# Performance work log

Measured on AMD Instinct MI355X. Metric: run time of the kernel, lower is better.

Reference implementation:

```python
import jax, jax.numpy as jnp
import numpy as np
import math

N = 200000      # active voxels
M = 100000      # matched in/out pairs per kernel offset
K = 27          # kernel volume (3x3x3)
CIN = 32
COUT = 64


def setup_inputs() -> dict:
    key = jax.random.key(0)
    k1, k2, k3, k4, k5 = jax.random.split(key, 5)
    input_feat = jax.random.normal(k1, (N, CIN), dtype=jnp.float32)
    input_coord = jax.random.randint(k2, (N, 4), 0, 1024, dtype=jnp.int32)
    input_cmap = jax.random.randint(k3, (N,), 0, N, dtype=jnp.int32)
    input_kmap = jax.random.randint(k4, (K, M, 2), 0, N, dtype=jnp.int32)
    std = 1.0 / math.sqrt(CIN * K)  # reset_parameters: uniform(-std, std)
    kw, kb = jax.random.split(k5)
    kernel = jax.random.uniform(kw, (K, CIN, COUT), dtype=jnp.float32,
                                minval=-std, maxval=std)
    bias = jax.random.uniform(kb, (COUT,), dtype=jnp.float32,
                              minval=-std, maxval=std)
    return {"input_feat": input_feat, "input_coord": input_coord,
            "input_cmap": input_cmap, "input_kmap": input_kmap,
            "kernel": kernel, "bias": bias}


def reference(input_feat, input_coord, input_cmap, input_kmap, kernel, bias):
    # Sparse 3D conv, stride=1: output coords == input coords, n_out = N.
    # For each kernel offset k, the kmap gives (in_idx, out_idx) pairs:
    #   out[out_idx] += in[in_idx] @ kernel[k]
    n_out = input_feat.shape[0]
    in_idx = input_kmap[..., 0]           # [K, M]
    out_idx = input_kmap[..., 1]          # [K, M]
    gathered = input_feat[in_idx]         # [K, M, CIN]  (gather)
    contrib = jnp.einsum('kmi,kio->kmo', gathered, kernel)  # per-offset GEMM
    out = jnp.zeros((n_out, kernel.shape[-1]), dtype=input_feat.dtype)
    out = out.at[out_idx.reshape(-1)].add(contrib.reshape(-1, kernel.shape[-1]))
    out = out + bias
    return out
```

## Files before the change

kernel.cpp:

```cpp
#include <hip/hip_runtime.h>
#include <stdint.h>

#define KVOL 27
#define CIN  32
#define COUT 64
#define RB16 16
#define WPG  4
#define ENTCAP 640
#define SCAN_CHUNK 4096

typedef __attribute__((ext_vector_type(8))) short bf16x8;
typedef __attribute__((ext_vector_type(4))) float f32x4;

__device__ __forceinline__ ushort f2bf(float f) {
  uint32_t u = __float_as_uint(f);
  u += 0x7FFFu + ((u >> 16) & 1u);
  return (ushort)(u >> 16);
}

__global__ __launch_bounds__(256) void kern_cvt_kernel(const float* __restrict__ kern,
                                                       ushort* __restrict__ kernT) {
  int tid = blockIdx.x * 256 + threadIdx.x;
  int kc   = tid & 3;
  int colq = (tid >> 2) & 15;
  int ct   = (tid >> 6) & 3;
  int ko   = tid >> 8;
  if (ko >= KVOL) return;
  const float* src = kern + (size_t)ko * CIN * COUT + ct * 16 + colq;
  ushort tmp[8];
#pragma unroll
  for (int j = 0; j < 8; ++j) tmp[j] = f2bf(src[(size_t)(kc * 8 + j) * COUT]);
  ushort* dst = kernT + (((size_t)(ko * 4 + ct) * 16 + colq) * 32 + kc * 8);
#pragma unroll
  for (int j = 0; j < 8; ++j) dst[j] = tmp[j];
}

__global__ __launch_bounds__(256) void hist_kernel(const int4* __restrict__ kmap2,
                                                   int* __restrict__ count, int M2) {
  int t = blockIdx.x * 256 + threadIdx.x;
  int k = blockIdx.y;
  if (t < M2) {
    int4 v = kmap2[(size_t)k * M2 + t];
    atomicAdd(&count[(v.y >> 4) * KVOL + k], 1);
    atomicAdd(&count[(v.w >> 4) * KVOL + k], 1);
  }
}

__global__ __launch_bounds__(256) void scan_reduce(const int* __restrict__ count,
                                                   int* __restrict__ partial, int nb) {
  __shared__ int ws[4];
  int t = threadIdx.x;
  int base = blockIdx.x * SCAN_CHUNK + t * 16;
  int s = 0;
#pragma unroll
  for (int i = 0; i < 16; ++i) { int idx = base + i; if (idx < nb) s += count[idx]; }
  for (int d = 32; d; d >>= 1) s += __shfl_down(s, d);
  if ((t & 63) == 0) ws[t >> 6] = s;
  __syncthreads();
  if (t == 0) partial[blockIdx.x] = ws[0] + ws[1] + ws[2] + ws[3];
}

__global__ __launch_bounds__(64) void scan_partials(int* __restrict__ partial,
                                                    int nchunks, int* __restrict__ total_out) {
  int lane = threadIdx.x;
  int run = 0;
  for (int base = 0; base < nchunks; base += 64) {
    int i = base + lane;
    int orig = (i < nchunks) ? partial[i] : 0;
    int v = orig;
    for (int d = 1; d < 64; d <<= 1) { int u = __shfl_up(v, d); if (lane >= d) v += u; }
    if (i < nchunks) partial[i] = run + v - orig;
    run += __shfl(v, 63);
  }
  if (lane == 0) *total_out = run;
}

__global__ __launch_bounds__(256) void scan_down(const int* __restrict__ count,
                                                 const int* __restrict__ partial,
                                                 int* __restrict__ start,
                                                 int* __restrict__ cursor, int nb) {
  __shared__ int wsum[4];
  int t = threadIdx.x, blk = blockIdx.x;
  int base = blk * SCAN_CHUNK + t * 16;
  int v[16]; int s = 0;
#pragma unroll
  for (int i = 0; i < 16; ++i) { int idx = base + i; v[i] = (idx < nb) ? count[idx] : 0; s += v[i]; }
  int lane = t & 63, wv = t >> 6;
  int sv = s;
  for (int d = 1; d < 64; d <<= 1) { int u = __shfl_up(sv, d); if (lane >= d) sv += u; }
  if (lane == 63) wsum[wv] = sv;
  __syncthreads();
  int wbase = 0;
  for (int i = 0; i < wv; ++i) wbase += wsum[i];
  int prefix = partial[blk] + wbase + (sv - s);
#pragma unroll
  for (int i = 0; i < 16; ++i) {
    int idx = base + i;
    if (idx < nb) { start[idx] = prefix; cursor[idx] = prefix; }
    prefix += v[i];
  }
}

__global__ __launch_bounds__(256) void scatter_kernel(const int4* __restrict__ kmap2,
                                                      int* __restrict__ cursor,
                                                      uint32_t* __restrict__ binned, int M2) {
  int t = blockIdx.x * 256 + threadIdx.x;
  int k = blockIdx.y;
  if (t < M2) {
    int4 v = kmap2[(size_t)k * M2 + t];
    int b1 = (v.y >> 4) * KVOL + k;
    int p1 = atomicAdd(&cursor[b1], 1);
    binned[p1] = (uint32_t)v.x | ((uint32_t)(v.y & 15) << 18);
    int b2 = (v.w >> 4) * KVOL + k;
    int p2 = atomicAdd(&cursor[b2], 1);
    binned[p2] = (uint32_t)v.z | ((uint32_t)(v.w & 15) << 18);
  }
}

#define STAGE(KK, OFF, CNT, G0, G1, RL, VAL) do {                              \
    int s_  = __shfl(sv, (KK));                                                \
    int s1_ = __shfl(sv, (KK) + 1);                                            \
    OFF = s_ - base0; CNT = s1_ - s_;                                          \
    int c0_ = CNT < 16 ? CNT : 16;                                             \
    VAL = (eidx < c0_);                                                        \
    uint32_t e_ = ents[wv][OFF + (VAL ? eidx : 0)];                            \
    RL = (int)(e_ >> 18);                                                      \
    const float* fp_ = feat + (size_t)(e_ & 0x3FFFFu) * CIN + part * 8;        \
    if (VAL) { G0 = *(const float4*)fp_; G1 = *(const float4*)(fp_ + 4); }     \
    else     { G0 = zf; G1 = zf; }                                             \
  } while (0)

#define CONSUME(KK, BUF, OFF, CNT, G0, G1, RL, VAL) do {                       \
    const ushort* kb_ = kernT + ((size_t)(KK) * 64 + q) * 32 + grp * 8;        \
    bf16x8 bf0_ = *(const bf16x8*)(kb_);                                       \
    bf16x8 bf1_ = *(const bf16x8*)(kb_ + 512);                                 \
    bf16x8 bf2_ = *(const bf16x8*)(kb_ + 1024);                                \
    bf16x8 bf3_ = *(const bf16x8*)(kb_ + 1536);                                \
    float* sp_ = &stage[wv][BUF][0][0];                                        \
    if (VAL) {                                                                 \
      float* rp_ = sp_ + RL * 36 + part * 8;                                   \
      atomicAdd(rp_ + 0, G0.x); atomicAdd(rp_ + 1, G0.y);                      \
      atomicAdd(rp_ + 2, G0.z); atomicAdd(rp_ + 3, G0.w);                      \
      atomicAdd(rp_ + 4, G1.x); atomicAdd(rp_ + 5, G1.y);                      \
      atomicAdd(rp_ + 6, G1.z); atomicAdd(rp_ + 7, G1.w);                      \
    }                                                                          \
    for (int off_ = 16; off_ < CNT; off_ += 16) {            \
      bool v_ = (off_ + eidx < CNT);                                           \
      uint32_t e_ = ents[wv][OFF + off_ + (v_ ? eidx : 0)];                    \
      if (v_) {                                                                \
        const float* fp_ = feat + (size_t)(e_ & 0x3FFFFu) * CIN + part * 8;    \
        float4 h0_ = *(const float4*)fp_;                                      \
        float4 h1_ = *(const float4*)(fp_ + 4);                                \
        float* rp_ = sp_ + (int)(e_ >> 18) * 36 + part * 8;                    \
        atomicAdd(rp_ + 0, h0_.x); atomicAdd(rp_ + 1, h0_.y);                  \
        atomicAdd(rp_ + 2, h0_.z); atomicAdd(rp_ + 3, h0_.w);                  \
        atomicAdd(rp_ + 4, h1_.x); atomicAdd(rp_ + 5, h1_.y);                  \
        atomicAdd(rp_ + 6, h1_.z); atomicAdd(rp_ + 7, h1_.w);                  \
      }                                                                        \
    }                                                                          \
    asm volatile("s_waitcnt lgkmcnt(0)" ::: "memory");                         \
    const float* ar_ = sp_ + q * 36 + grp * 8;                                 \
    float4 u0_ = *(const float4*)ar_;                                          \
    float4 u1_ = *(const float4*)(ar_ + 4);                                    \
    bf16x8 af_;                                                                \
    af_[0] = (short)f2bf(u0_.x); af_[1] = (short)f2bf(u0_.y);                  \
    af_[2] = (short)f2bf(u0_.z); af_[3] = (short)f2bf(u0_.w);                  \
    af_[4] = (short)f2bf(u1_.x); af_[5] = (short)f2bf(u1_.y);                  \
    af_[6] = (short)f2bf(u1_.z); af_[7] = (short)f2bf(u1_.w);                  \
    acc0 = __builtin_amdgcn_mfma_f32_16x16x32_bf16(af_, bf0_, acc0, 0, 0, 0);  \
    acc1 = __builtin_amdgcn_mfma_f32_16x16x32_bf16(af_, bf1_, acc1, 0, 0, 0);  \
    acc2 = __builtin_amdgcn_mfma_f32_16x16x32_bf16(af_, bf2_, acc2, 0, 0, 0);  \
    acc3 = __builtin_amdgcn_mfma_f32_16x16x32_bf16(af_, bf3_, acc3, 0, 0, 0);  \
    asm volatile("s_waitcnt lgkmcnt(0)" ::: "memory");                         \
    float2* zp_ = (float2*)sp_;                                                \
    zp_[l] = z2; zp_[l + 64] = z2; zp_[l + 128] = z2;                          \
    if (l < 32) zp_[l + 256] = z2;                                             \
    zp_[l + 192] = z2;                                                         \
  } while (0)

__global__ __launch_bounds__(256, 4) void conv_mfma2(
    const float* __restrict__ feat,
    const uint32_t* __restrict__ binned,
    const int* __restrict__ start,
    const ushort* __restrict__ kernT,
    const float* __restrict__ bias,
    float* __restrict__ out) {
  __shared__ float stage[WPG][2][RB16][36];
  __shared__ uint32_t ents[WPG][ENTCAP];
  const int wv  = threadIdx.x >> 6;
  const int l   = threadIdx.x & 63;
  const int q   = l & 15;
  const int grp = l >> 4;
  const int eidx = l >> 2;
  const int part = l & 3;
  const int blk = blockIdx.x * WPG + wv;
  const float4 zf = {0.f, 0.f, 0.f, 0.f};
  const float2 z2 = {0.f, 0.f};

  int sv = 0;
  if (l <= KVOL) sv = start[blk * KVOL + l];
  const int base0 = __shfl(sv, 0);
  int total = __shfl(sv, KVOL) - base0;
  if (total > ENTCAP) total = ENTCAP;

  for (int i = l; i < total; i += 64) ents[wv][i] = binned[base0 + i];

  {
    float2* zp = (float2*)&stage[wv][0][0][0];
#pragma unroll
    for (int i = 0; i < 9; ++i) zp[l + i * 64] = z2;
  }

  float bv0 = bias[q], bv1 = bias[16 + q], bv2 = bias[32 + q], bv3 = bias[48 + q];

  asm volatile("s_waitcnt lgkmcnt(0)" ::: "memory");

  f32x4 acc0 = {0,0,0,0}, acc1 = {0,0,0,0}, acc2 = {0,0,0,0}, acc3 = {0,0,0,0};
  int offA, cntA, rlA; bool valA; float4 gA0, gA1;
  int offB, cntB, rlB; bool valB; float4 gB0, gB1;

  STAGE(0, offA, cntA, gA0, gA1, rlA, valA);
  for (int k = 0; k < KVOL - 1; k += 2) {
    STAGE(k + 1, offB, cntB, gB0, gB1, rlB, valB);
    CONSUME(k, 0, offA, cntA, gA0, gA1, rlA, valA);
    STAGE(k + 2, offA, cntA, gA0, gA1, rlA, valA);
    CONSUME(k + 1, 1, offB, cntB, gB0, gB1, rlB, valB);
  }
  CONSUME(KVOL - 1, 0, offA, cntA, gA0, gA1, rlA, valA);

  const int R0 = blk * RB16;
#pragma unroll
  for (int reg = 0; reg < 4; ++reg) {
    float* op = out + (size_t)(R0 + grp * 4 + reg) * COUT + q;
    op[0]  = acc0[reg] + bv0;
    op[16] = acc1[reg] + bv1;
    op[32] = acc2[reg] + bv2;
    op[48] = acc3[reg] + bv3;
  }
}

extern "C" void kernel_launch(void* const* d_in, const int* in_sizes, int n_in,
                              void* d_out, int out_size, void* d_ws, size_t ws_size,
                              hipStream_t stream) {
  const float* feat = (const float*)d_in[0];
  const int4*  kmap2 = (const int4*)d_in[3];
  const float* kern = (const float*)d_in[4];
  const float* bias = (const float*)d_in[5];
  float* out = (float*)d_out;

  const int N = in_sizes[0] / CIN;
  const int M = in_sizes[3] / (2 * KVOL);
  const int M2 = M / 2;
  const int NBLK16 = N / RB16;
  const int NBIN = NBLK16 * KVOL;

  ushort* kernT = (ushort*)d_ws;
  int* count    = (int*)(kernT + (size_t)KVOL * CIN * COUT);
  int* startA   = count + NBIN;
  int* cursor   = startA + NBIN + 1;
  int* partial  = cursor + NBIN;
  uint32_t* binned = (uint32_t*)(partial + 128);

  const int nchunks = (NBIN + SCAN_CHUNK - 1) / SCAN_CHUNK;

  hipMemsetAsync(count, 0, (size_t)NBIN * sizeof(int), stream);
  hipLaunchKernelGGL(kern_cvt_kernel, dim3(KVOL), dim3(256), 0, stream, kern, kernT);

  dim3 pgrid((M2 + 255) / 256, KVOL);
  hipLaunchKernelGGL(hist_kernel, pgrid, dim3(256), 0, stream, kmap2, count, M2);
  hipLaunchKernelGGL(scan_reduce, dim3(nchunks), dim3(256), 0, stream, count, partial, NBIN);
  hipLaunchKernelGGL(scan_partials, dim3(1), dim3(64), 0, stream, partial, nchunks, startA + NBIN);
  hipLaunchKernelGGL(scan_down, dim3(nchunks), dim3(256), 0, stream,
                     count, partial, startA, cursor, NBIN);
  hipLaunchKernelGGL(scatter_kernel, pgrid, dim3(256), 0, stream, kmap2, cursor, binned, M2);

  hipLaunchKernelGGL(conv_mfma2, dim3(NBLK16 / WPG), dim3(256), 0, stream,
                     feat, binned, startA, kernT, bias, out);
}
```

Measured before the change: 809.8 us.

## Pre-convert features to bf16 and reorder bins offset-major for coalesced scatter

```diff
diff --git a/kernel.cpp b/kernel.cpp
--- a/kernel.cpp
+++ b/kernel.cpp
@@ -6,16 +6,35 @@
 #define COUT 64
 #define RB16 16
 #define WPG  4
-#define ENTCAP 640
+#define ENTCAP 384
 #define SCAN_CHUNK 4096
 
 typedef __attribute__((ext_vector_type(8))) short bf16x8;
+typedef __attribute__((ext_vector_type(8))) ushort u16x8;
 typedef __attribute__((ext_vector_type(4))) float f32x4;
 
 __device__ __forceinline__ ushort f2bf(float f) {
   uint32_t u = __float_as_uint(f);
   u += 0x7FFFu + ((u >> 16) & 1u);
   return (ushort)(u >> 16);
+}
+
+__device__ __forceinline__ uint32_t cvtpk(float lo, float hi) {
+  uint32_t r;
+  asm("v_cvt_pk_bf16_f32 %0, %1, %2" : "=v"(r) : "v"(lo), "v"(hi));
+  return r;
+}
+
+__global__ __launch_bounds__(256) void feat_cvt_kernel(const float* __restrict__ feat,
+                                                       ushort* __restrict__ feat16,
+                                                       int total4) {
+  int i = blockIdx.x * 256 + threadIdx.x;
+  if (i < total4) {
+    float4 v = ((const float4*)feat)[i];
+    ushort4 o;
+    o.x = f2bf(v.x); o.y = f2bf(v.y); o.z = f2bf(v.z); o.w = f2bf(v.w);
+    ((ushort4*)feat16)[i] = o;
+  }
 }
 
 __global__ __launch_bounds__(256) void kern_cvt_kernel(const float* __restrict__ kern,
@@ -36,13 +55,14 @@
 }
 
 __global__ __launch_bounds__(256) void hist_kernel(const int4* __restrict__ kmap2,
-                                                   int* __restrict__ count, int M2) {
+                                                   int* __restrict__ count,
+                                                   int M2, int NB) {
   int t = blockIdx.x * 256 + threadIdx.x;
   int k = blockIdx.y;
   if (t < M2) {
     int4 v = kmap2[(size_t)k * M2 + t];
-    atomicAdd(&count[(v.y >> 4) * KVOL + k], 1);
-    atomicAdd(&count[(v.w >> 4) * KVOL + k], 1);
+    atomicAdd(&count[k * NB + (v.y >> 4)], 1);
+    atomicAdd(&count[k * NB + (v.w >> 4)], 1);
   }
 }
 
@@ -103,59 +123,59 @@
 
 __global__ __launch_bounds__(256) void scatter_kernel(const int4* __restrict__ kmap2,
                                                       int* __restrict__ cursor,
-                                                      uint32_t* __restrict__ binned, int M2) {
+                                                      uint32_t* __restrict__ binned,
+                                                      int M2, int NB) {
   int t = blockIdx.x * 256 + threadIdx.x;
   int k = blockIdx.y;
   if (t < M2) {
     int4 v = kmap2[(size_t)k * M2 + t];
-    int b1 = (v.y >> 4) * KVOL + k;
-    int p1 = atomicAdd(&cursor[b1], 1);
+    int p1 = atomicAdd(&cursor[k * NB + (v.y >> 4)], 1);
     binned[p1] = (uint32_t)v.x | ((uint32_t)(v.y & 15) << 18);
-    int b2 = (v.w >> 4) * KVOL + k;
-    int p2 = atomicAdd(&cursor[b2], 1);
+    int p2 = atomicAdd(&cursor[k * NB + (v.w >> 4)], 1);
     binned[p2] = (uint32_t)v.z | ((uint32_t)(v.w & 15) << 18);
   }
 }
 
-#define STAGE(KK, OFF, CNT, G0, G1, RL, VAL) do {                              \
-    int s_  = __shfl(sv, (KK));                                                \
-    int s1_ = __shfl(sv, (KK) + 1);                                            \
-    OFF = s_ - base0; CNT = s1_ - s_;                                          \
+#define STAGE(KK, OFF, CNT, G, RL, VAL) do {                                   \
+    OFF = __shfl(excl, (KK));                                                  \
+    CNT = __shfl(cnt_l, (KK));                                                 \
     int c0_ = CNT < 16 ? CNT : 16;                                             \
     VAL = (eidx < c0_);                                                        \
-    uint32_t e_ = ents[wv][OFF + (VAL ? eidx : 0)];                            \
-    RL = (int)(e_ >> 18);                                                      \
-    const float* fp_ = feat + (size_t)(e_ & 0x3FFFFu) * CIN + part * 8;        \
-    if (VAL) { G0 = *(const float4*)fp_; G1 = *(const float4*)(fp_ + 4); }     \
-    else     { G0 = zf; G1 = zf; }                                             \
+    int ix_ = OFF + (VAL ? eidx : 0);                                          \
+    if (ix_ >= ENTCAP) ix_ = 0;                                                \
+    uint32_t e_ = ents[wv][ix_];                                               \
+    RL = (int)((e_ >> 18) & 15u);                                              \
+    const ushort* fp_ = feat16 + (size_t)(e_ & 0x3FFFFu) * CIN + part * 8;     \
+    if (VAL) G = *(const u16x8*)fp_;                                           \
   } while (0)
 
-#define CONSUME(KK, BUF, OFF, CNT, G0, G1, RL, VAL) do {                       \
+#define PRESUM8(G_, RLX, PARTX) do {                                           \
+    float* rp_ = sp_ + (RLX) * 36 + (PARTX) * 8;                               \
+    _Pragma("unroll")                                                          \
+    for (int j_ = 0; j_ < 8; ++j_) {                                           \
+      float fv_ = __uint_as_float((uint32_t)(ushort)(G_)[j_] << 16);           \
+      atomicAdd(rp_ + j_, fv_);                                                \
+    }                                                                          \
+  } while (0)
+
+#define CONSUME(KK, BUF, OFF, CNT, G, RL, VAL) do {                            \
     const ushort* kb_ = kernT + ((size_t)(KK) * 64 + q) * 32 + grp * 8;        \
     bf16x8 bf0_ = *(const bf16x8*)(kb_);                                       \
     bf16x8 bf1_ = *(const bf16x8*)(kb_ + 512);                                 \
     bf16x8 bf2_ = *(const bf16x8*)(kb_ + 1024);                                \
     bf16x8 bf3_ = *(const bf16x8*)(kb_ + 1536);                                \
     float* sp_ = &stage[wv][BUF][0][0];                                        \
-    if (VAL) {                                                                 \
-      float* rp_ = sp_ + RL * 36 + part * 8;                                   \
-      atomicAdd(rp_ + 0, G0.x); atomicAdd(rp_ + 1, G0.y);                      \
-      atomicAdd(rp_ + 2, G0.z); atomicAdd(rp_ + 3, G0.w);                      \
-      atomicAdd(rp_ + 4, G1.x); atomicAdd(rp_ + 5, G1.y);                      \
-      atomicAdd(rp_ + 6, G1.z); atomicAdd(rp_ + 7, G1.w);                      \
-    }                                                                          \
+    if (VAL) PRESUM8(G, RL, part);                                             \
     for (int off_ = 16; off_ < CNT; off_ += 16) {            \
       bool v_ = (off_ + eidx < CNT);                                           \
-      uint32_t e_ = ents[wv][OFF + off_ + (v_ ? eidx : 0)];                    \
+      int ixT_ = OFF + off_ + (v_ ? eidx : 0);                                 \
+      if (ixT_ >= ENTCAP) ixT_ = 0;                                            \
+      uint32_t e_ = ents[wv][ixT_];                                            \
       if (v_) {                                                                \
-        const float* fp_ = feat + (size_t)(e_ & 0x3FFFFu) * CIN + part * 8;    \
-        float4 h0_ = *(const float4*)fp_;                                      \
-        float4 h1_ = *(const float4*)(fp_ + 4);                                \
-        float* rp_ = sp_ + (int)(e_ >> 18) * 36 + part * 8;                    \
-        atomicAdd(rp_ + 0, h0_.x); atomicAdd(rp_ + 1, h0_.y);                  \
-        atomicAdd(rp_ + 2, h0_.z); atomicAdd(rp_ + 3, h0_.w);                  \
-        atomicAdd(rp_ + 4, h1_.x); atomicAdd(rp_ + 5, h1_.y);                  \
-        atomicAdd(rp_ + 6, h1_.z); atomicAdd(rp_ + 7, h1_.w);                  \
+        const ushort* fpT_ = feat16 + (size_t)(e_ & 0x3FFFFu) * CIN + part * 8;\
+        u16x8 h_ = *(const u16x8*)fpT_;                                        \
+        int rlT_ = (int)((e_ >> 18) & 15u);                                    \
+        PRESUM8(h_, rlT_, part);                                               \
       }                                                                        \
     }                                                                          \
     asm volatile("s_waitcnt lgkmcnt(0)" ::: "memory");                         \
@@ -163,10 +183,12 @@
     float4 u0_ = *(const float4*)ar_;                                          \
     float4 u1_ = *(const float4*)(ar_ + 4);                                    \
     bf16x8 af_;                                                                \
-    af_[0] = (short)f2bf(u0_.x); af_[1] = (short)f2bf(u0_.y);                  \
-    af_[2] = (short)f2bf(u0_.z); af_[3] = (short)f2bf(u0_.w);                  \
-    af_[4] = (short)f2bf(u1_.x); af_[5] = (short)f2bf(u1_.y);                  \
-    af_[6] = (short)f2bf(u1_.z); af_[7] = (short)f2bf(u1_.w);                  \
+    uint32_t w0_ = cvtpk(u0_.x, u0_.y), w1_ = cvtpk(u0_.z, u0_.w);             \
+    uint32_t w2_ = cvtpk(u1_.x, u1_.y), w3_ = cvtpk(u1_.z, u1_.w);             \
+    af_[0] = (short)(w0_ & 0xFFFF); af_[1] = (short)(w0_ >> 16);               \
+    af_[2] = (short)(w1_ & 0xFFFF); af_[3] = (short)(w1_ >> 16);               \
+    af_[4] = (short)(w2_ & 0xFFFF); af_[5] = (short)(w2_ >> 16);               \
+    af_[6] = (short)(w3_ & 0xFFFF); af_[7] = (short)(w3_ >> 16);               \
     acc0 = __builtin_amdgcn_mfma_f32_16x16x32_bf16(af_, bf0_, acc0, 0, 0, 0);  \
     acc1 = __builtin_amdgcn_mfma_f32_16x16x32_bf16(af_, bf1_, acc1, 0, 0, 0);  \
     acc2 = __builtin_amdgcn_mfma_f32_16x16x32_bf16(af_, bf2_, acc2, 0, 0, 0);  \
@@ -174,17 +196,18 @@
     asm volatile("s_waitcnt lgkmcnt(0)" ::: "memory");                         \
     float2* zp_ = (float2*)sp_;                                                \
     zp_[l] = z2; zp_[l + 64] = z2; zp_[l + 128] = z2;                          \
+    zp_[l + 192] = z2;                                                         \
     if (l < 32) zp_[l + 256] = z2;                                             \
-    zp_[l + 192] = z2;                                                         \
   } while (0)
 
-__global__ __launch_bounds__(256, 4) void conv_mfma2(
-    const float* __restrict__ feat,
+__global__ __launch_bounds__(256, 4) void conv_mfma7(
+    const ushort* __restrict__ feat16,
     const uint32_t* __restrict__ binned,
     const int* __restrict__ start,
     const ushort* __restrict__ kernT,
     const float* __restrict__ bias,
-    float* __restrict__ out) {
+    float* __restrict__ out,
+    int NB) {
   __shared__ float stage[WPG][2][RB16][36];
   __shared__ uint32_t ents[WPG][ENTCAP];
   const int wv  = threadIdx.x >> 6;
@@ -194,16 +217,26 @@
   const int eidx = l >> 2;
   const int part = l & 3;
   const int blk = blockIdx.x * WPG + wv;
-  const float4 zf = {0.f, 0.f, 0.f, 0.f};
   const float2 z2 = {0.f, 0.f};
 
-  int sv = 0;
-  if (l <= KVOL) sv = start[blk * KVOL + l];
-  const int base0 = __shfl(sv, 0);
-  int total = __shfl(sv, KVOL) - base0;
-  if (total > ENTCAP) total = ENTCAP;
-
-  for (int i = l; i < total; i += 64) ents[wv][i] = binned[base0 + i];
+  int s_lo = 0, s_hi = 0;
+  if (l < KVOL) {
+    s_lo = start[l * NB + blk];
+    s_hi = start[l * NB + blk + 1];
+  }
+  int cnt_l = s_hi - s_lo;
+  int pfx = cnt_l;
+#pragma unroll
+  for (int d = 1; d < 32; d <<= 1) { int u = __shfl_up(pfx, d); if (l >= d) pfx += u; }
+  int excl = pfx - cnt_l;
+  if (excl + cnt_l > ENTCAP) cnt_l = 0;
+
+  for (int j = 0; j < KVOL; ++j) {
+    int sj = __shfl(s_lo, j);
+    int cj = __shfl(cnt_l, j);
+    int oj = __shfl(excl, j);
+    for (int i = l; i < cj; i += 64) ents[wv][oj + i] = binned[sj + i];
+  }
 
   {
     float2* zp = (float2*)&stage[wv][0][0][0];
@@ -214,19 +247,20 @@
   float bv0 = bias[q], bv1 = bias[16 + q], bv2 = bias[32 + q], bv3 = bias[48 + q];
 
   asm volatile("s_waitcnt lgkmcnt(0)" ::: "memory");
+  __builtin_amdgcn_sched_barrier(0);
 
   f32x4 acc0 = {0,0,0,0}, acc1 = {0,0,0,0}, acc2 = {0,0,0,0}, acc3 = {0,0,0,0};
-  int offA, cntA, rlA; bool valA; float4 gA0, gA1;
-  int offB, cntB, rlB; bool valB; float4 gB0, gB1;
-
-  STAGE(0, offA, cntA, gA0, gA1, rlA, valA);
+  int offA, cntA, rlA; bool valA; u16x8 gA = {0,0,0,0,0,0,0,0};
+  int offB, cntB, rlB; bool valB; u16x8 gB = {0,0,0,0,0,0,0,0};
+
+  STAGE(0, offA, cntA, gA, rlA, valA);
   for (int k = 0; k < KVOL - 1; k += 2) {
-    STAGE(k + 1, offB, cntB, gB0, gB1, rlB, valB);
-    CONSUME(k, 0, offA, cntA, gA0, gA1, rlA, valA);
-    STAGE(k + 2, offA, cntA, gA0, gA1, rlA, valA);
-    CONSUME(k + 1, 1, offB, cntB, gB0, gB1, rlB, valB);
-  }
-  CONSUME(KVOL - 1, 0, offA, cntA, gA0, gA1, rlA, valA);
+    STAGE(k + 1, offB, cntB, gB, rlB, valB);
+    CONSUME(k, 0, offA, cntA, gA, rlA, valA);
+    STAGE(k + 2, offA, cntA, gA, rlA, valA);
+    CONSUME(k + 1, 1, offB, cntB, gB, rlB, valB);
+  }
+  CONSUME(KVOL - 1, 0, offA, cntA, gA, rlA, valA);
 
   const int R0 = blk * RB16;
 #pragma unroll
@@ -242,38 +276,41 @@
 extern "C" void kernel_launch(void* const* d_in, const int* in_sizes, int n_in,
                               void* d_out, int out_size, void* d_ws, size_t ws_size,
                               hipStream_t stream) {
-  const float* feat = (const float*)d_in[0];
+  const float* feat  = (const float*)d_in[0];
   const int4*  kmap2 = (const int4*)d_in[3];
-  const float* kern = (const float*)d_in[4];
-  const float* bias = (const float*)d_in[5];
+  const float* kern  = (const float*)d_in[4];
+  const float* bias  = (const float*)d_in[5];
   float* out = (float*)d_out;
 
   const int N = in_sizes[0] / CIN;
   const int M = in_sizes[3] / (2 * KVOL);
   const int M2 = M / 2;
-  const int NBLK16 = N / RB16;
-  const int NBIN = NBLK16 * KVOL;
-
-  ushort* kernT = (ushort*)d_ws;
-  int* count    = (int*)(kernT + (size_t)KVOL * CIN * COUT);
-  int* startA   = count + NBIN;
-  int* cursor   = startA + NBIN + 1;
-  int* partial  = cursor + NBIN;
+  const int NB = N / RB16;
+  const int NBIN = NB * KVOL;
+
+  ushort* feat16 = (ushort*)d_ws;
+  ushort* kernT  = feat16 + (size_t)N * CIN;
+  int* count   = (int*)(kernT + (size_t)KVOL * CIN * COUT);
+  int* startA  = count + NBIN;
+  int* cursor  = startA + NBIN + 1;
+  int* partial = cursor + NBIN;
   uint32_t* binned = (uint32_t*)(partial + 128);
 
   const int nchunks = (NBIN + SCAN_CHUNK - 1) / SCAN_CHUNK;
 
   hipMemsetAsync(count, 0, (size_t)NBIN * sizeof(int), stream);
+  hipLaunchKernelGGL(feat_cvt_kernel, dim3((N * CIN / 4 + 255) / 256), dim3(256), 0, stream,
+                     feat, feat16, N * CIN / 4);
   hipLaunchKernelGGL(kern_cvt_kernel, dim3(KVOL), dim3(256), 0, stream, kern, kernT);
 
   dim3 pgrid((M2 + 255) / 256, KVOL);
-  hipLaunchKernelGGL(hist_kernel, pgrid, dim3(256), 0, stream, kmap2, count, M2);
+  hipLaunchKernelGGL(hist_kernel, pgrid, dim3(256), 0, stream, kmap2, count, M2, NB);
   hipLaunchKernelGGL(scan_reduce, dim3(nchunks), dim3(256), 0, stream, count, partial, NBIN);
   hipLaunchKernelGGL(scan_partials, dim3(1), dim3(64), 0, stream, partial, nchunks, startA + NBIN);
   hipLaunchKernelGGL(scan_down, dim3(nchunks), dim3(256), 0, stream,
                      count, partial, startA, cursor, NBIN);
-  hipLaunchKernelGGL(scatter_kernel, pgrid, dim3(256), 0, stream, kmap2, cursor, binned, M2);
-
-  hipLaunchKernelGGL(conv_mfma2, dim3(NBLK16 / WPG), dim3(256), 0, stream,
-                     feat, binned, startA, kernT, bias, out);
-}
+  hipLaunchKernelGGL(scatter_kernel, pgrid, dim3(256), 0, stream, kmap2, cursor, binned, M2, NB);
+
+  hipLaunchKernelGGL(conv_mfma7, dim3(NB / WPG), dim3(256), 0, stream,
+                     feat16, binned, startA, kernT, bias, out, NB);
+}
```

Result: no change. 810.2 us (+0.1%).
